# Kernel optimization log

Hardware: AMD Instinct MI355X
Metric: run time of the kernel (lower is better)

The kernel has to match this reference:

```python
import jax, jax.numpy as jnp
import numpy as np

# Block structure (mirrors init_kwargs)
K = 8            # number of blocks
BLK = 1024       # per-block in/out width
TOTAL = K * BLK  # total_dim = 8192
INPUT_IDX = [(i * BLK, (i + 1) * BLK) for i in range(K)]
OUTPUT_IDX = [(((i + 1) % K) * BLK, ((i + 1) % K + 1) * BLK) for i in range(K)]
BATCH = 4096


def setup_inputs() -> dict:
    key = jax.random.key(0)
    k1, k2, k3, k4 = jax.random.split(key, 4)
    x = jax.random.normal(k1, (BATCH, TOTAL), dtype=jnp.float32)
    v = jax.random.normal(k2, (BATCH, TOTAL), dtype=jnp.float32)
    # Per-block Linear params; nn.Linear default init ~ U(-1/sqrt(in), 1/sqrt(in))
    bound = 1.0 / np.sqrt(BLK)
    W = jax.random.uniform(k3, (K, BLK, BLK), dtype=jnp.float32, minval=-bound, maxval=bound)  # [K, out, in]
    b = jax.random.uniform(k4, (K, BLK), dtype=jnp.float32, minval=-bound, maxval=bound)
    return {"x": x, "v": v, "W": W, "b": b}


def reference(x, v, W, b):
    # hidden = act(v)
    hidden = jnp.tanh(v)
    # All input blocks are a uniform partition -> batch the K small GEMMs as one grouped contraction.
    h = hidden.reshape(BATCH, K, BLK)                      # [B, K, in]
    y = jnp.einsum("bki,koi->bko", h, W) + b               # [B, K, out]
    # Scatter-accumulate each block output into its padded position, plus residual x.
    result = x
    for i, (o0, o1) in enumerate(OUTPUT_IDX):
        result = result.at[:, o0:o1].add(y[:, i])
    return result
```

## Files before the change

### kernel.cpp

```cpp
#include <hip/hip_runtime.h>
#include <hip/hip_bf16.h>
#include <stdint.h>

#define BATCH 4096
#define KGRP  8
#define BLK   1024
#define TOTAL 8192

#define BM 128
#define BN 128
#define BK 32

typedef __attribute__((ext_vector_type(8))) short short8;
typedef __attribute__((ext_vector_type(4))) float f32x4;


__device__ __forceinline__ unsigned short f2bf(float f) {
    union { float f; uint32_t u; } c; c.f = f;
    uint32_t u = c.u;
    u += 0x7fffu + ((u >> 16) & 1u);
    return (unsigned short)(u >> 16);
}

__device__ __forceinline__ float fast_tanh(float x) {
    float e = __expf(2.0f * x);
    return 1.0f - 2.0f / (e + 1.0f);
}

__device__ __forceinline__ uint32_t swz(uint32_t p) {
    return p ^ (((p >> 7) & 3u) << 4);
}


__global__ void k_tanh_cast(const float4* __restrict__ v, ushort4* __restrict__ H) {
    const int n4 = BATCH * TOTAL / 4;
    int i = blockIdx.x * blockDim.x + threadIdx.x;
    const int stride = gridDim.x * blockDim.x;
    for (; i < n4; i += stride) {
        float4 f = v[i];
        ushort4 o;
        o.x = f2bf(fast_tanh(f.x));
        o.y = f2bf(fast_tanh(f.y));
        o.z = f2bf(fast_tanh(f.z));
        o.w = f2bf(fast_tanh(f.w));
        H[i] = o;
    }
}

__global__ void k_wcast(const float4* __restrict__ W, ushort4* __restrict__ Wb) {
    const int n4 = KGRP * BLK * BLK / 4;
    int i = blockIdx.x * blockDim.x + threadIdx.x;
    const int stride = gridDim.x * blockDim.x;
    for (; i < n4; i += stride) {
        float4 f = W[i];
        ushort4 o;
        o.x = f2bf(f.x); o.y = f2bf(f.y); o.z = f2bf(f.z); o.w = f2bf(f.w);
        Wb[i] = o;
    }
}


__global__ __launch_bounds__(256, 2)
void k_gemm(const unsigned short* __restrict__ H, const unsigned short* __restrict__ Wb,
            const float* __restrict__ x, const float* __restrict__ bias,
            float* __restrict__ out) {
    __shared__ __attribute__((aligned(16))) unsigned short As[BM * BK];
    __shared__ __attribute__((aligned(16))) unsigned short Bs[BN * BK];

    const int h = blockIdx.x;
    const int flat = (h & 7) * 256 + (h >> 3);
    const int g = flat >> 8;
    const int mtile = (flat >> 3) & 31;
    const int ntile = flat & 7;

    const int tid = threadIdx.x;
    const int lane = tid & 63;
    const int w = tid >> 6;
    const int wr = w >> 1, wc = w & 1;

    int rS[2], cS[2];
#pragma unroll
    for (int s = 0; s < 2; ++s) {
        uint32_t p = (uint32_t)(s * 4096 + tid * 16);
        uint32_t q = swz(p);
        rS[s] = (int)(q >> 6);
        cS[s] = (int)((q & 63u) >> 1);
    }
    const unsigned short* Abase = H  + (size_t)(mtile * BM) * TOTAL + (size_t)g * BLK;
    const unsigned short* Bbase = Wb + ((size_t)g * BLK + (size_t)ntile * BN) * BLK;
    const uint32_t ldsWaveBase = (uint32_t)(w << 10);

    uint32_t aoff[4], boff[4];
#pragma unroll
    for (int m = 0; m < 4; ++m) {
        uint32_t row = (uint32_t)(wr * 64 + m * 16 + (lane & 15));
        aoff[m] = swz(row * 64u + (uint32_t)(lane >> 4) * 16u);
    }
#pragma unroll
    for (int n = 0; n < 4; ++n) {
        uint32_t row = (uint32_t)(wc * 64 + n * 16 + (lane & 15));
        boff[n] = swz(row * 64u + (uint32_t)(lane >> 4) * 16u);
    }

    f32x4 acc[4][4];
#pragma unroll
    for (int m = 0; m < 4; ++m)
#pragma unroll
        for (int n = 0; n < 4; ++n) acc[m][n] = (f32x4){0.f, 0.f, 0.f, 0.f};

    const char* AsB = (const char*)As;
    const char* BsB = (const char*)Bs;

    for (int kt = 0; kt < BLK / BK; ++kt) {
        const unsigned short* Ak = Abase + kt * BK;
        const unsigned short* Bk = Bbase + kt * BK;
#pragma unroll
        for (int s = 0; s < 2; ++s) {
            __builtin_amdgcn_global_load_lds(
                (const __attribute__((address_space(1))) uint32_t*)(Ak + (size_t)rS[s] * TOTAL + cS[s]),
                (__attribute__((address_space(3))) uint32_t*)((char*)As + s * 4096 + ldsWaveBase),
                16, 0, 0);
            __builtin_amdgcn_global_load_lds(
                (const __attribute__((address_space(1))) uint32_t*)(Bk + (size_t)rS[s] * BLK + cS[s]),
                (__attribute__((address_space(3))) uint32_t*)((char*)Bs + s * 4096 + ldsWaveBase),
                16, 0, 0);
        }
        __syncthreads();

        short8 af[4], bf8[4];
#pragma unroll
        for (int m = 0; m < 4; ++m) af[m] = *(const short8*)(AsB + aoff[m]);
#pragma unroll
        for (int n = 0; n < 4; ++n) bf8[n] = *(const short8*)(BsB + boff[n]);
#pragma unroll
        for (int m = 0; m < 4; ++m)
#pragma unroll
            for (int n = 0; n < 4; ++n)
                acc[m][n] = __builtin_amdgcn_mfma_f32_16x16x32_bf16(af[m], bf8[n], acc[m][n], 0, 0, 0);
        __syncthreads();
    }

    const int gout = (g + 1) & 7;
    const int row0 = mtile * BM + wr * 64 + ((lane >> 4) << 2);
    const int col0 = ntile * BN + wc * 64 + (lane & 15);
    float bv[4];
#pragma unroll
    for (int n = 0; n < 4; ++n) bv[n] = bias[g * BLK + col0 + n * 16];
#pragma unroll
    for (int m = 0; m < 4; ++m) {
#pragma unroll
        for (int j = 0; j < 4; ++j) {
            const int row = row0 + m * 16 + j;
            const size_t base = (size_t)row * TOTAL + (size_t)gout * BLK;
#pragma unroll
            for (int n = 0; n < 4; ++n) {
                const size_t idx = base + col0 + n * 16;
                out[idx] = x[idx] + bv[n] + acc[m][n][j];
            }
        }
    }
}


__global__ void k_naive(const float* __restrict__ x, const float* __restrict__ v,
                        const float* __restrict__ W, const float* __restrict__ b,
                        float* __restrict__ out) {
    __shared__ float hv[BLK];
    const int bid = blockIdx.x;
    const int quarter = bid & 3;
    const int g = (bid >> 2) & 7;
    const int row = bid >> 5;
    for (int i = threadIdx.x; i < BLK; i += 256)
        hv[i] = tanhf(v[(size_t)row * TOTAL + g * BLK + i]);
    __syncthreads();
    const int o = quarter * 256 + threadIdx.x;
    const float* wrow = W + ((size_t)g * BLK + o) * BLK;
    float s = 0.f;
    for (int i = 0; i < BLK; ++i) s += hv[i] * wrow[i];
    const size_t oi = (size_t)row * TOTAL + (size_t)((g + 1) & 7) * BLK + o;
    out[oi] = x[oi] + b[g * BLK + o] + s;
}


extern "C" void kernel_launch(void* const* d_in, const int* in_sizes, int n_in,
                              void* d_out, int out_size, void* d_ws, size_t ws_size,
                              hipStream_t stream) {
    const float* x = (const float*)d_in[0];
    const float* v = (const float*)d_in[1];
    const float* W = (const float*)d_in[2];
    const float* b = (const float*)d_in[3];
    float* out = (float*)d_out;

    const size_t needH = (size_t)BATCH * TOTAL * sizeof(unsigned short);
    const size_t needW = (size_t)KGRP * BLK * BLK * sizeof(unsigned short);

    if (ws_size >= needH + needW) {
        unsigned short* H  = (unsigned short*)d_ws;
        unsigned short* Wb = (unsigned short*)((char*)d_ws + needH);
        k_tanh_cast<<<2048, 256, 0, stream>>>((const float4*)v, (ushort4*)H);
        k_wcast<<<1024, 256, 0, stream>>>((const float4*)W, (ushort4*)Wb);
        k_gemm<<<2048, 256, 0, stream>>>(H, Wb, x, b, out);
    } else {
        k_naive<<<BATCH * KGRP * 4, 256, 0, stream>>>(x, v, W, b, out);
    }
}
```

Measured before the change: 165.8 us.

## Rewrite grouped GEMM with 256x256 tiles, double-buffered LDS and phased MFMA scheduling

Result: faster. 161.0 us (-2.9%).

```diff
diff --git a/kernel.cpp b/kernel.cpp
--- a/kernel.cpp
+++ b/kernel.cpp
@@ -6,10 +6,6 @@
 #define KGRP  8
 #define BLK   1024
 #define TOTAL 8192
-
-#define BM 128
-#define BN 128
-#define BK 32
 
 typedef __attribute__((ext_vector_type(8))) short short8;
 typedef __attribute__((ext_vector_type(4))) float f32x4;
@@ -25,10 +21,6 @@
 __device__ __forceinline__ float fast_tanh(float x) {
     float e = __expf(2.0f * x);
     return 1.0f - 2.0f / (e + 1.0f);
-}
-
-__device__ __forceinline__ uint32_t swz(uint32_t p) {
-    return p ^ (((p >> 7) & 3u) << 4);
 }
 
 
@@ -60,101 +52,169 @@
 }
 
 
-__global__ __launch_bounds__(256, 2)
+__global__ __launch_bounds__(512, 2)
 void k_gemm(const unsigned short* __restrict__ H, const unsigned short* __restrict__ Wb,
             const float* __restrict__ x, const float* __restrict__ bias,
             float* __restrict__ out) {
-    __shared__ __attribute__((aligned(16))) unsigned short As[BM * BK];
-    __shared__ __attribute__((aligned(16))) unsigned short Bs[BN * BK];
-
-    const int h = blockIdx.x;
-    const int flat = (h & 7) * 256 + (h >> 3);
-    const int g = flat >> 8;
-    const int mtile = (flat >> 3) & 31;
-    const int ntile = flat & 7;
-
-    const int tid = threadIdx.x;
+    __shared__ __attribute__((aligned(1024))) char lds[131072];
+
+    const int bid   = blockIdx.x;
+    const int g     = bid & 7;
+    const int slot  = bid >> 3;
+    const int mtile = slot >> 2;
+    const int ntile = slot & 3;
+
+    const int tid  = threadIdx.x;
     const int lane = tid & 63;
-    const int w = tid >> 6;
-    const int wr = w >> 1, wc = w & 1;
-
-    int rS[2], cS[2];
-#pragma unroll
-    for (int s = 0; s < 2; ++s) {
-        uint32_t p = (uint32_t)(s * 4096 + tid * 16);
-        uint32_t q = swz(p);
-        rS[s] = (int)(q >> 6);
-        cS[s] = (int)((q & 63u) >> 1);
-    }
-    const unsigned short* Abase = H  + (size_t)(mtile * BM) * TOTAL + (size_t)g * BLK;
-    const unsigned short* Bbase = Wb + ((size_t)g * BLK + (size_t)ntile * BN) * BLK;
-    const uint32_t ldsWaveBase = (uint32_t)(w << 10);
-
-    uint32_t aoff[4], boff[4];
-#pragma unroll
-    for (int m = 0; m < 4; ++m) {
-        uint32_t row = (uint32_t)(wr * 64 + m * 16 + (lane & 15));
-        aoff[m] = swz(row * 64u + (uint32_t)(lane >> 4) * 16u);
-    }
-#pragma unroll
-    for (int n = 0; n < 4; ++n) {
-        uint32_t row = (uint32_t)(wc * 64 + n * 16 + (lane & 15));
-        boff[n] = swz(row * 64u + (uint32_t)(lane >> 4) * 16u);
-    }
-
-    f32x4 acc[4][4];
-#pragma unroll
-    for (int m = 0; m < 4; ++m)
+    const int w    = tid >> 6;
+    const int wr   = w >> 2;
+    const int wc   = w & 3;
+
+    const uint32_t flip  = (uint32_t)(((lane >> 2) & 1) << 5);
+    const uint32_t kcol  = ((uint32_t)((lane >> 4) * 16)) ^ flip;
+    const uint32_t aBase = (uint32_t)(wr * 128 + (lane & 15)) * 128u + kcol;
+    const uint32_t bBase = 32768u + (uint32_t)(wc * 64 + (lane & 15)) * 128u + kcol;
+
+    const int sRow = tid >> 3;
+    const int sCol = ((tid & 7) * 8) ^ (((tid >> 5) & 1) << 4);
+    const unsigned short* Asrc0 = H  + ((size_t)(mtile * 256) + sRow) * TOTAL + (size_t)g * BLK + sCol;
+    const unsigned short* Bsrc0 = Wb + ((size_t)g * BLK * BLK) + ((size_t)(ntile * 256) + sRow) * BLK + sCol;
+    const uint32_t ldsStageBase = (uint32_t)(w << 10);
+
+    auto stageA = [&](int kt, uint32_t bufb) {
+#pragma unroll
+        for (int c = 0; c < 4; ++c)
+            __builtin_amdgcn_global_load_lds(
+                (const __attribute__((address_space(1))) uint32_t*)(Asrc0 + (size_t)(c * 64) * TOTAL + kt * 64),
+                (__attribute__((address_space(3))) uint32_t*)(lds + bufb + c * 8192 + ldsStageBase),
+                16, 0, 0);
+    };
+    auto stageB = [&](int kt, uint32_t bufb) {
+#pragma unroll
+        for (int c = 0; c < 4; ++c)
+            __builtin_amdgcn_global_load_lds(
+                (const __attribute__((address_space(1))) uint32_t*)(Bsrc0 + (size_t)(c * 64) * BLK + kt * 64),
+                (__attribute__((address_space(3))) uint32_t*)(lds + bufb + 32768u + c * 8192 + ldsStageBase),
+                16, 0, 0);
+    };
+
+    f32x4 acc[8][4];
+#pragma unroll
+    for (int m = 0; m < 8; ++m)
 #pragma unroll
         for (int n = 0; n < 4; ++n) acc[m][n] = (f32x4){0.f, 0.f, 0.f, 0.f};
 
-    const char* AsB = (const char*)As;
-    const char* BsB = (const char*)Bs;
-
-    for (int kt = 0; kt < BLK / BK; ++kt) {
-        const unsigned short* Ak = Abase + kt * BK;
-        const unsigned short* Bk = Bbase + kt * BK;
-#pragma unroll
-        for (int s = 0; s < 2; ++s) {
-            __builtin_amdgcn_global_load_lds(
-                (const __attribute__((address_space(1))) uint32_t*)(Ak + (size_t)rS[s] * TOTAL + cS[s]),
-                (__attribute__((address_space(3))) uint32_t*)((char*)As + s * 4096 + ldsWaveBase),
-                16, 0, 0);
-            __builtin_amdgcn_global_load_lds(
-                (const __attribute__((address_space(1))) uint32_t*)(Bk + (size_t)rS[s] * BLK + cS[s]),
-                (__attribute__((address_space(3))) uint32_t*)((char*)Bs + s * 4096 + ldsWaveBase),
-                16, 0, 0);
-        }
-        __syncthreads();
-
-        short8 af[4], bf8[4];
-#pragma unroll
-        for (int m = 0; m < 4; ++m) af[m] = *(const short8*)(AsB + aoff[m]);
-#pragma unroll
-        for (int n = 0; n < 4; ++n) bf8[n] = *(const short8*)(BsB + boff[n]);
-#pragma unroll
-        for (int m = 0; m < 4; ++m)
-#pragma unroll
-            for (int n = 0; n < 4; ++n)
-                acc[m][n] = __builtin_amdgcn_mfma_f32_16x16x32_bf16(af[m], bf8[n], acc[m][n], 0, 0, 0);
-        __syncthreads();
+    stageA(0, 0u);
+    stageB(0, 0u);
+    asm volatile("s_waitcnt vmcnt(0)" ::: "memory");
+    __builtin_amdgcn_s_barrier();
+    __builtin_amdgcn_sched_barrier(0);
+
+    uint32_t cur = 0;
+    for (int kt = 0; kt < 16; ++kt) {
+        const uint32_t bufb = cur << 16;
+        const uint32_t nbuf = bufb ^ 65536u;
+        const char* Lb = lds + bufb;
+        const bool st = (kt < 15);
+
+        short8 bfr[4][2];
+        short8 am[2][2];
+
+#pragma unroll
+        for (int n = 0; n < 4; ++n)
+#pragma unroll
+            for (int ks = 0; ks < 2; ++ks)
+                bfr[n][ks] = *(const short8*)(Lb + bBase + n * 2048 + ks * 64);
+#pragma unroll
+        for (int i = 0; i < 2; ++i)
+#pragma unroll
+            for (int ks = 0; ks < 2; ++ks)
+                am[i][ks] = *(const short8*)(Lb + aBase + (0 + i) * 2048 + ks * 64);
+        if (st) stageA(kt + 1, nbuf);
+        __builtin_amdgcn_s_barrier();
+        __builtin_amdgcn_s_setprio(1);
+#pragma unroll
+        for (int i = 0; i < 2; ++i)
+#pragma unroll
+            for (int n = 0; n < 4; ++n)
+#pragma unroll
+                for (int ks = 0; ks < 2; ++ks)
+                    acc[0 + i][n] = __builtin_amdgcn_mfma_f32_16x16x32_bf16(am[i][ks], bfr[n][ks], acc[0 + i][n], 0, 0, 0);
+        __builtin_amdgcn_s_setprio(0);
+        __builtin_amdgcn_s_barrier();
+
+#pragma unroll
+        for (int i = 0; i < 2; ++i)
+#pragma unroll
+            for (int ks = 0; ks < 2; ++ks)
+                am[i][ks] = *(const short8*)(Lb + aBase + (2 + i) * 2048 + ks * 64);
+        if (st) stageB(kt + 1, nbuf);
+        __builtin_amdgcn_s_barrier();
+        __builtin_amdgcn_s_setprio(1);
+#pragma unroll
+        for (int i = 0; i < 2; ++i)
+#pragma unroll
+            for (int n = 0; n < 4; ++n)
+#pragma unroll
+                for (int ks = 0; ks < 2; ++ks)
+                    acc[2 + i][n] = __builtin_amdgcn_mfma_f32_16x16x32_bf16(am[i][ks], bfr[n][ks], acc[2 + i][n], 0, 0, 0);
+        __builtin_amdgcn_s_setprio(0);
+        __builtin_amdgcn_s_barrier();
+
+#pragma unroll
+        for (int i = 0; i < 2; ++i)
+#pragma unroll
+            for (int ks = 0; ks < 2; ++ks)
+                am[i][ks] = *(const short8*)(Lb + aBase + (4 + i) * 2048 + ks * 64);
+        __builtin_amdgcn_s_barrier();
+        __builtin_amdgcn_s_setprio(1);
+#pragma unroll
+        for (int i = 0; i < 2; ++i)
+#pragma unroll
+            for (int n = 0; n < 4; ++n)
+#pragma unroll
+                for (int ks = 0; ks < 2; ++ks)
+                    acc[4 + i][n] = __builtin_amdgcn_mfma_f32_16x16x32_bf16(am[i][ks], bfr[n][ks], acc[4 + i][n], 0, 0, 0);
+        __builtin_amdgcn_s_setprio(0);
+        __builtin_amdgcn_s_barrier();
+
+#pragma unroll
+        for (int i = 0; i < 2; ++i)
+#pragma unroll
+            for (int ks = 0; ks < 2; ++ks)
+                am[i][ks] = *(const short8*)(Lb + aBase + (6 + i) * 2048 + ks * 64);
+        __builtin_amdgcn_s_barrier();
+        __builtin_amdgcn_s_setprio(1);
+#pragma unroll
+        for (int i = 0; i < 2; ++i)
+#pragma unroll
+            for (int n = 0; n < 4; ++n)
+#pragma unroll
+                for (int ks = 0; ks < 2; ++ks)
+                    acc[6 + i][n] = __builtin_amdgcn_mfma_f32_16x16x32_bf16(am[i][ks], bfr[n][ks], acc[6 + i][n], 0, 0, 0);
+        __builtin_amdgcn_s_setprio(0);
+
+        asm volatile("s_waitcnt vmcnt(0)" ::: "memory");
+        __builtin_amdgcn_s_barrier();
+        __builtin_amdgcn_sched_barrier(0);
+        cur ^= 1u;
     }
 
     const int gout = (g + 1) & 7;
-    const int row0 = mtile * BM + wr * 64 + ((lane >> 4) << 2);
-    const int col0 = ntile * BN + wc * 64 + (lane & 15);
+    const int row0 = mtile * 256 + wr * 128 + ((lane >> 4) << 2);
+    const int colL = ntile * 256 + wc * 64 + (lane & 15);
     float bv[4];
 #pragma unroll
-    for (int n = 0; n < 4; ++n) bv[n] = bias[g * BLK + col0 + n * 16];
-#pragma unroll
-    for (int m = 0; m < 4; ++m) {
+    for (int n = 0; n < 4; ++n) bv[n] = bias[g * BLK + colL + n * 16];
+#pragma unroll
+    for (int m = 0; m < 8; ++m) {
 #pragma unroll
         for (int j = 0; j < 4; ++j) {
             const int row = row0 + m * 16 + j;
             const size_t base = (size_t)row * TOTAL + (size_t)gout * BLK;
 #pragma unroll
             for (int n = 0; n < 4; ++n) {
-                const size_t idx = base + col0 + n * 16;
+                const size_t idx = base + colL + n * 16;
                 out[idx] = x[idx] + bv[n] + acc[m][n][j];
             }
         }
@@ -199,7 +259,7 @@
         unsigned short* Wb = (unsigned short*)((char*)d_ws + needH);
         k_tanh_cast<<<2048, 256, 0, stream>>>((const float4*)v, (ushort4*)H);
         k_wcast<<<1024, 256, 0, stream>>>((const float4*)W, (ushort4*)Wb);
-        k_gemm<<<2048, 256, 0, stream>>>(H, Wb, x, b, out);
+        k_gemm<<<512, 512, 0, stream>>>(H, Wb, x, b, out);
     } else {
         k_naive<<<BATCH * KGRP * 4, 256, 0, stream>>>(x, v, W, b, out);
     }
```
